# Optimization experiments

Measured on AMD Instinct MI355X. Metric: run time of the kernel, lower is better.

## Reference

```python
import jax, jax.numpy as jnp
import numpy as np

B, C, E, H = 4, 2048, 1024, 16
D = E // H
EPS = 1e-5

def _layernorm(x, g, b):
    mu = jnp.mean(x, axis=-1, keepdims=True)
    var = jnp.mean(jnp.square(x - mu), axis=-1, keepdims=True)
    return (x - mu) * jax.lax.rsqrt(var + EPS) * g + b

def setup_inputs() -> dict:
    key = jax.random.key(0)
    ks = jax.random.split(key, 12)
    s = 1.0 / np.sqrt(E)
    return {
        "inputs": jax.random.normal(ks[0], (B, C, E), dtype=jnp.float32),
        "Wq": jax.random.normal(ks[1], (E, E), dtype=jnp.float32) * s,
        "bq": jnp.zeros((E,), dtype=jnp.float32),
        "Wk": jax.random.normal(ks[2], (E, E), dtype=jnp.float32) * s,
        "bk": jnp.zeros((E,), dtype=jnp.float32),
        "Wv": jax.random.normal(ks[3], (E, E), dtype=jnp.float32) * s,
        "bv": jnp.zeros((E,), dtype=jnp.float32),
        "g1": jnp.ones((E,), dtype=jnp.float32),
        "beta1": jnp.zeros((E,), dtype=jnp.float32),
        "g2": jnp.ones((E,), dtype=jnp.float32),
        "beta2": jnp.zeros((E,), dtype=jnp.float32),
        "W1": jax.random.normal(ks[4], (E, 4 * E), dtype=jnp.float32) * s,
        "bm1": jnp.zeros((4 * E,), dtype=jnp.float32),
        "W2": jax.random.normal(ks[5], (4 * E, E), dtype=jnp.float32) * (1.0 / np.sqrt(4 * E)),
        "bm2": jnp.zeros((E,), dtype=jnp.float32),
    }

def reference(inputs, Wq, bq, Wk, bk, Wv, bv, g1, beta1, g2, beta2, W1, bm1, W2, bm2):
    b, c, e = inputs.shape
    normed = _layernorm(inputs, g1, beta1)
    q = (normed @ Wq + bq).reshape(b, c, H, D).transpose(0, 2, 1, 3)  # [B,H,C,D]
    k = (normed @ Wk + bk).reshape(b, c, H, D).transpose(0, 2, 1, 3)
    v = (normed @ Wv + bv).reshape(b, c, H, D).transpose(0, 2, 1, 3)
    scores = jnp.einsum('bhqd,bhkd->bhqk', q, k) / np.sqrt(D).astype(np.float32)
    causal = jnp.triu(jnp.ones((c, c), dtype=bool), k=1)  # True above diagonal
    scores = jnp.where(causal, -jnp.inf, scores)
    probs = jax.nn.softmax(scores, axis=-1)
    attn = jnp.einsum('bhqk,bhkd->bhqd', probs, v)
    attn = attn.transpose(0, 2, 1, 3).reshape(b, c, e)
    out = inputs + attn
    h = _layernorm(out, g2, beta2)
    mlp = jax.nn.relu(h @ W1 + bm1) @ W2 + bm2
    return out + mlp
```

## Files before the change

kernel.cpp:

```cpp
#include <hip/hip_runtime.h>
#include <math.h>

#define B_ 4
#define C_ 2048
#define E_ 1024
#define H_ 16
#define D_ 64
#define ROWS_ (B_*C_)

typedef __bf16 bf16x8 __attribute__((ext_vector_type(8)));
typedef float f32x4 __attribute__((ext_vector_type(4)));

__device__ __forceinline__ float b2f(unsigned short u) {
  unsigned int x = ((unsigned int)u) << 16;
  return __builtin_bit_cast(float, x);
}
__device__ __forceinline__ unsigned short f2b(float f) {
  unsigned int x = __builtin_bit_cast(unsigned int, f);
  unsigned int r = (x + 0x7FFFu + ((x >> 16) & 1u)) >> 16;
  return (unsigned short)r;
}
__device__ __forceinline__ unsigned short tob(float f) { return f2b(f); }
__device__ __forceinline__ unsigned short tob(unsigned short u) { return u; }
__device__ __forceinline__ void store_out(float* p, float v) { *p = v; }
__device__ __forceinline__ void store_out(unsigned short* p, float v) { *p = f2b(v); }

__device__ __forceinline__ void async16(const void* g, void* l) {
  __builtin_amdgcn_global_load_lds(
      (__attribute__((address_space(1))) unsigned int*)g,
      (__attribute__((address_space(3))) unsigned int*)l, 16, 0, 0);
}

template <typename InT>
__global__ __launch_bounds__(256) void transpose64(
    const InT* __restrict__ in, unsigned short* __restrict__ out,
    int s_in, int s_out, int Hz, long zs_b, long zs_h, long zs_out)
{
  __shared__ unsigned short t[64][65];
  int z = blockIdx.z;
  long ib = (long)(z / Hz) * zs_b + (long)(z % Hz) * zs_h;
  long ob = (long)z * zs_out;
  int r0 = blockIdx.y * 64, c0 = blockIdx.x * 64;
  int lane = threadIdx.x & 63, grp = threadIdx.x >> 6;
  for (int i = grp; i < 64; i += 4)
    t[i][lane] = tob(in[ib + (long)(r0 + i) * s_in + c0 + lane]);
  __syncthreads();
  for (int i = grp; i < 64; i += 4)
    out[ob + (long)(c0 + i) * s_out + r0 + lane] = t[lane][i];
}

__global__ void concat_bias(const float* __restrict__ q,
                            const float* __restrict__ k,
                            const float* __restrict__ v,
                            float* __restrict__ o)
{
  int i = blockIdx.x * 256 + threadIdx.x;
  o[i] = (i < 1024) ? q[i] : (i < 2048) ? k[i - 1024] : v[i - 2048];
}

__global__ __launch_bounds__(256) void ln_kernel(
    const float* __restrict__ xin, const unsigned short* __restrict__ addend,
    const float* __restrict__ g, const float* __restrict__ beta,
    unsigned short* __restrict__ yout, float* __restrict__ out1)
{
  int row = blockIdx.x, tid = threadIdx.x;
  size_t base = (size_t)row * E_ + tid * 4;
  float4 xa = *(const float4*)(xin + base);
  float v0 = xa.x, v1 = xa.y, v2 = xa.z, v3 = xa.w;
  if (addend) {
    ushort4 aa = *(const ushort4*)(addend + base);
    v0 += b2f(aa.x); v1 += b2f(aa.y); v2 += b2f(aa.z); v3 += b2f(aa.w);
  }
  if (out1) {
    *(float4*)(out1 + base) = make_float4(v0, v1, v2, v3);
  }
  float s = v0 + v1 + v2 + v3;
  float sq = v0*v0 + v1*v1 + v2*v2 + v3*v3;
  #pragma unroll
  for (int off = 32; off >= 1; off >>= 1) {
    s  += __shfl_xor(s, off);
    sq += __shfl_xor(sq, off);
  }
  __shared__ float red[8];
  int wid = tid >> 6;
  if ((tid & 63) == 0) { red[wid] = s; red[4 + wid] = sq; }
  __syncthreads();
  s  = red[0] + red[1] + red[2] + red[3];
  sq = red[4] + red[5] + red[6] + red[7];
  float mu = s * (1.0f / E_);
  float var = sq * (1.0f / E_) - mu * mu;
  float rs = rsqrtf(var + 1e-5f);
  float4 ga = *(const float4*)(g + tid * 4);
  float4 ba = *(const float4*)(beta + tid * 4);
  ushort4 o;
  o.x = f2b((v0 - mu) * rs * ga.x + ba.x);
  o.y = f2b((v1 - mu) * rs * ga.y + ba.y);
  o.z = f2b((v2 - mu) * rs * ga.z + ba.z);
  o.w = f2b((v3 - mu) * rs * ga.w + ba.w);
  *(ushort4*)(yout + base) = o;
}

template <typename OutT>
__global__ __launch_bounds__(256) void gemm_bt(
    const unsigned short* __restrict__ A, const unsigned short* __restrict__ Bt,
    const float* __restrict__ bias, const float* __restrict__ resid,
    OutT* __restrict__ Co, int M, int N, int K, int lda, int ldb,
    int relu, size_t zs)
{
  __shared__ __align__(16) unsigned short As[128 * 64];
  __shared__ __align__(16) unsigned short Bs[128 * 64];
  int tid = threadIdx.x, lane = tid & 63, wid = tid >> 6;
  int lane15 = lane & 15, quad = lane >> 4;

  int i = blockIdx.x;
  int xcd = i & 7, s = i >> 3;
  int bn = s >> 3;
  int bm = xcd * 8 + (s & 7);
  size_t koff = (size_t)blockIdx.z * K;
  int z0 = (blockIdx.z == 0);
  Co += (size_t)blockIdx.z * zs;

  int m_lo = (wid & 1) * 64, n_lo = (wid >> 1) * 64;

  f32x4 acc[4][4];
  #pragma unroll
  for (int a = 0; a < 4; ++a)
    #pragma unroll
    for (int bb = 0; bb < 4; ++bb) acc[a][bb] = 0.0f;

  int sr = tid >> 3, sc = tid & 7;
  int scs = (sc ^ (sr & 7)) * 8;
  const unsigned short* Ag = A + koff + (size_t)(bm * 128 + sr) * lda + scs;
  const unsigned short* Bg = Bt + koff + (size_t)(bn * 128 + sr) * ldb + scs;
  unsigned short* Al = &As[wid * 512];
  unsigned short* Bl = &Bs[wid * 512];
  int sw15 = lane15 & 7;

  for (int k0 = 0; k0 < K; k0 += 64) {
    async16(Ag,                     Al);
    async16(Ag + (size_t)32 * lda,  Al + 32 * 64);
    async16(Ag + (size_t)64 * lda,  Al + 64 * 64);
    async16(Ag + (size_t)96 * lda,  Al + 96 * 64);
    async16(Bg,                     Bl);
    async16(Bg + (size_t)32 * ldb,  Bl + 32 * 64);
    async16(Bg + (size_t)64 * ldb,  Bl + 64 * 64);
    async16(Bg + (size_t)96 * ldb,  Bl + 96 * 64);
    Ag += 64; Bg += 64;
    __syncthreads();

    #pragma unroll
    for (int kk = 0; kk < 2; ++kk) {
      bf16x8 af[4], bfr[4];
      int qs = kk * 4 + quad;
      #pragma unroll
      for (int t = 0; t < 4; ++t)
        af[t] = *(const bf16x8*)&As[(m_lo + t * 16 + lane15) * 64 + ((qs ^ sw15) * 8)];
      #pragma unroll
      for (int t = 0; t < 4; ++t)
        bfr[t] = *(const bf16x8*)&Bs[(n_lo + t * 16 + lane15) * 64 + ((qs ^ sw15) * 8)];
      #pragma unroll
      for (int mt = 0; mt < 4; ++mt)
        #pragma unroll
        for (int nt = 0; nt < 4; ++nt)
          acc[mt][nt] = __builtin_amdgcn_mfma_f32_16x16x32_bf16(af[mt], bfr[nt], acc[mt][nt], 0, 0, 0);
    }
    __syncthreads();
  }

  #pragma unroll
  for (int nt = 0; nt < 4; ++nt) {
    int col = bn * 128 + n_lo + nt * 16 + lane15;
    float bv = (bias && z0) ? bias[col] : 0.0f;
    #pragma unroll
    for (int mt = 0; mt < 4; ++mt) {
      int row0 = bm * 128 + m_lo + mt * 16 + quad * 4;
      #pragma unroll
      for (int r = 0; r < 4; ++r) {
        float val = acc[mt][nt][r] + bv;
        if (relu) val = fmaxf(val, 0.0f);
        if (resid && z0) val += resid[(size_t)(row0 + r) * N + col];
        store_out(&Co[(size_t)(row0 + r) * N + col], val);
      }
    }
  }
}

__global__ __launch_bounds__(256) void add2(
    const float* __restrict__ p0, const float* __restrict__ p1,
    float* __restrict__ out)
{
  size_t i = ((size_t)blockIdx.x * 256 + threadIdx.x) * 4;
  float4 a = *(const float4*)(p0 + i);
  float4 b = *(const float4*)(p1 + i);
  *(float4*)(out + i) = make_float4(a.x + b.x, a.y + b.y, a.z + b.z, a.w + b.w);
}

__global__ __launch_bounds__(512) void attn_kernel(
    const unsigned short* __restrict__ qkv, const unsigned short* __restrict__ vt,
    unsigned short* __restrict__ attnb,
    float* __restrict__ opart0, float* __restrict__ opart1,
    float* __restrict__ lpart)
{
  __shared__ __align__(16) unsigned short Klds[64 * 64];
  __shared__ __align__(16) unsigned short Vlds[64 * 64];
  __shared__ __align__(16) unsigned short Plds[8][16 * 72];
  int tid = threadIdx.x, lane = tid & 63, widx = tid >> 6;
  int lane15 = lane & 15, quad = lane >> 4;

  int bx = blockIdx.x;
  int qblk, p, split;
  if (bx < 16) { qblk = 15 - (bx >> 1); p = bx & 1; split = 1; }
  else         { qblk = 23 - bx;        p = 0;      split = 0; }
  int ntiles = 2 * qblk + 2;
  int kt0 = (split && p) ? (qblk + 1) : 0;
  int kt1 = (split && !p) ? (qblk + 1) : ntiles;

  int bh = blockIdx.y;
  int b = bh >> 4, h = bh & 15;
  int q0w = qblk * 128 + widx * 16;

  const float QSCALE = 0.18033688011112042f;
  const unsigned short* qb = qkv + (size_t)(b * C_ + q0w + lane15) * 3072 + h * 64;
  bf16x8 qa0 = *(const bf16x8*)(qb + quad * 8);
  bf16x8 qa1 = *(const bf16x8*)(qb + 32 + quad * 8);
  #pragma unroll
  for (int j = 0; j < 8; ++j) {
    qa0[j] = (__bf16)((float)qa0[j] * QSCALE);
    qa1[j] = (__bf16)((float)qa1[j] * QSCALE);
  }

  float lsum[4];
  f32x4 o[4];
  #pragma unroll
  for (int r = 0; r < 4; ++r) lsum[r] = 0.0f;
  #pragma unroll
  for (int nt = 0; nt < 4; ++nt) o[nt] = 0.0f;

  int sr = tid >> 3, sc = tid & 7, sw = sr & 7;
  const unsigned short* kg = qkv + (size_t)(b * C_ + kt0 * 64 + sr) * 3072 + 1024 + h * 64 + (sc ^ sw) * 8;
  const unsigned short* vg = vt + (size_t)bh * 64 * 2048 + (size_t)sr * 2048 + (sc ^ sw) * 8 + kt0 * 64;
  unsigned short* kl = &Klds[sr * 64 + sc * 8];
  unsigned short* vl = &Vlds[sr * 64 + sc * 8];
  int swr = lane15 & 7;

  for (int kt = kt0; kt < kt1; ++kt) {
    int k0 = kt * 64;
    async16(kg, kl);
    async16(vg, vl);
    kg += (size_t)64 * 3072;
    vg += 64;
    __syncthreads();

    if (k0 <= q0w + 15) {
      f32x4 s[4];
      #pragma unroll
      for (int g = 0; g < 4; ++g) s[g] = 0.0f;
      #pragma unroll
      for (int g = 0; g < 4; ++g) {
        int row = g * 16 + lane15;
        bf16x8 kf0 = *(const bf16x8*)&Klds[row * 64 + ((quad ^ swr) * 8)];
        bf16x8 kf1 = *(const bf16x8*)&Klds[row * 64 + (((4 + quad) ^ swr) * 8)];
        s[g] = __builtin_amdgcn_mfma_f32_16x16x32_bf16(qa0, kf0, s[g], 0, 0, 0);
        s[g] = __builtin_amdgcn_mfma_f32_16x16x32_bf16(qa1, kf1, s[g], 0, 0, 0);
      }

      if (k0 + 63 > q0w) {
        #pragma unroll
        for (int g = 0; g < 4; ++g)
          #pragma unroll
          for (int r = 0; r < 4; ++r)
            if (k0 + g * 16 + lane15 > q0w + quad * 4 + r) s[g][r] = -3.0e38f;
      }

      float pv[4][4];
      #pragma unroll
      for (int g = 0; g < 4; ++g)
        #pragma unroll
        for (int r = 0; r < 4; ++r) pv[g][r] = exp2f(s[g][r]);
      #pragma unroll
      for (int r = 0; r < 4; ++r)
        lsum[r] += (pv[0][r] + pv[1][r]) + (pv[2][r] + pv[3][r]);

      __bf16* prow = (__bf16*)&Plds[widx][0];
      #pragma unroll
      for (int g = 0; g < 4; ++g)
        #pragma unroll
        for (int r = 0; r < 4; ++r)
          prow[(quad * 4 + r) * 72 + g * 16 + lane15] = (__bf16)pv[g][r];
      asm volatile("s_waitcnt lgkmcnt(0)" ::: "memory");
      bf16x8 pa0 = *(const bf16x8*)&Plds[widx][lane15 * 72 + quad * 8];
      bf16x8 pa1 = *(const bf16x8*)&Plds[widx][lane15 * 72 + 32 + quad * 8];

      #pragma unroll
      for (int nt = 0; nt < 4; ++nt) {
        int d = nt * 16 + lane15;
        bf16x8 vf0 = *(const bf16x8*)&Vlds[d * 64 + ((quad ^ swr) * 8)];
        bf16x8 vf1 = *(const bf16x8*)&Vlds[d * 64 + (((4 + quad) ^ swr) * 8)];
        o[nt] = __builtin_amdgcn_mfma_f32_16x16x32_bf16(pa0, vf0, o[nt], 0, 0, 0);
        o[nt] = __builtin_amdgcn_mfma_f32_16x16x32_bf16(pa1, vf1, o[nt], 0, 0, 0);
      }
    }
    __syncthreads();
  }

  #pragma unroll
  for (int off = 1; off <= 8; off <<= 1)
    #pragma unroll
    for (int r = 0; r < 4; ++r)
      lsum[r] += __shfl_xor(lsum[r], off);

  if (!split) {
    float rl[4];
    #pragma unroll
    for (int r = 0; r < 4; ++r) rl[r] = 1.0f / lsum[r];
    #pragma unroll
    for (int nt = 0; nt < 4; ++nt)
      #pragma unroll
      for (int r = 0; r < 4; ++r) {
        float val = o[nt][r] * rl[r];
        attnb[(size_t)(b * C_ + q0w + quad * 4 + r) * E_ + h * 64 + nt * 16 + lane15] = f2b(val);
      }
  } else {
    float* op = p ? opart1 : opart0;
    size_t rbase = (size_t)bh * 1024 + (q0w - 1024) + quad * 4;
    #pragma unroll
    for (int nt = 0; nt < 4; ++nt)
      #pragma unroll
      for (int r = 0; r < 4; ++r)
        op[(rbase + r) * 64 + nt * 16 + lane15] = o[nt][r];
    if (lane15 == 0) {
      float* lp = lpart + (size_t)p * 65536;
      #pragma unroll
      for (int r = 0; r < 4; ++r) lp[rbase + r] = lsum[r];
    }
  }
}

__global__ __launch_bounds__(256) void attn_combine(
    const float* __restrict__ opart0, const float* __restrict__ opart1,
    const float* __restrict__ lpart, unsigned short* __restrict__ attnb)
{
  size_t i = (size_t)blockIdx.x * 256 + threadIdx.x;
  int d = (int)(i & 63);
  size_t rowi = i >> 6;
  int bh = (int)(rowi >> 10), row = (int)(rowi & 1023);
  float ov = opart0[rowi * 64 + d] + opart1[rowi * 64 + d];
  float lv = lpart[rowi] + lpart[65536 + rowi];
  int b = bh >> 4, h = bh & 15;
  attnb[(size_t)(b * C_ + 1024 + row) * E_ + h * 64 + d] = f2b(ov / lv);
}

extern "C" void kernel_launch(void* const* d_in, const int* in_sizes, int n_in,
                              void* d_out, int out_size, void* d_ws, size_t ws_size,
                              hipStream_t stream)
{
  const float* x   = (const float*)d_in[0];
  const float* Wq  = (const float*)d_in[1];
  const float* bq  = (const float*)d_in[2];
  const float* Wk  = (const float*)d_in[3];
  const float* bk  = (const float*)d_in[4];
  const float* Wv  = (const float*)d_in[5];
  const float* bv  = (const float*)d_in[6];
  const float* g1  = (const float*)d_in[7];
  const float* be1 = (const float*)d_in[8];
  const float* g2  = (const float*)d_in[9];
  const float* be2 = (const float*)d_in[10];
  const float* W1  = (const float*)d_in[11];
  const float* bm1 = (const float*)d_in[12];
  const float* W2  = (const float*)d_in[13];
  const float* bm2 = (const float*)d_in[14];

  char* ws = (char*)d_ws;
  float*          part0 = (float*)(ws + 0);
  unsigned short* norm1 = (unsigned short*)(ws + 0);
  unsigned short* wT    = (unsigned short*)(ws + 16777216);
  unsigned short* w1T   = (unsigned short*)(ws + 23068672);
  float*          biasq = (float*)(ws + 39845888);
  unsigned short* qkv   = (unsigned short*)(ws + 39858176);
  unsigned short* vtb   = (unsigned short*)(ws + 90189824);
  unsigned short* mid   = (unsigned short*)(ws + 39858176);
  unsigned short* attnb = (unsigned short*)(ws + 106967040);
  float*          out1  = (float*)(ws + 123744256);
  unsigned short* w2T   = (unsigned short*)(ws + 157298688);
  float*          part1 = (float*)(ws + 165687296);
  float*          opart0 = (float*)(ws + 165687296);
  float*          opart1 = (float*)(ws + 123744256);
  float*          lpartb = (float*)(ws + 0);
  size_t part_zs = ((size_t)165687296) / 4;

  transpose64<float><<<dim3(16, 16, 1), 256, 0, stream>>>(Wq, wT,               1024, 1024, 1, 0, 0, 0);
  transpose64<float><<<dim3(16, 16, 1), 256, 0, stream>>>(Wk, wT + 1024 * 1024, 1024, 1024, 1, 0, 0, 0);
  transpose64<float><<<dim3(16, 16, 1), 256, 0, stream>>>(Wv, wT + 2048 * 1024, 1024, 1024, 1, 0, 0, 0);
  transpose64<float><<<dim3(64, 16, 1), 256, 0, stream>>>(W1, w1T, 4096, 1024, 1, 0, 0, 0);
  transpose64<float><<<dim3(16, 64, 1), 256, 0, stream>>>(W2, w2T, 1024, 4096, 1, 0, 0, 0);
  concat_bias<<<12, 256, 0, stream>>>(bq, bk, bv, biasq);

  ln_kernel<<<ROWS_, 256, 0, stream>>>(x, nullptr, g1, be1, norm1, nullptr);

  gemm_bt<unsigned short><<<dim3(24 * 64, 1, 1), 256, 0, stream>>>(
      norm1, wT, biasq, nullptr, qkv, 8192, 3072, 1024, 1024, 1024, 0, 0);

  transpose64<unsigned short><<<dim3(1, 32, 64), 256, 0, stream>>>(
      qkv + 2048, vtb, 3072, 2048, 16, (long)C_ * 3072, 64, (long)64 * 2048);

  attn_kernel<<<dim3(24, 64), 512, 0, stream>>>(qkv, vtb, attnb, opart0, opart1, lpartb);
  attn_combine<<<16384, 256, 0, stream>>>(opart0, opart1, lpartb, attnb);

  ln_kernel<<<ROWS_, 256, 0, stream>>>(x, attnb, g2, be2, norm1, out1);

  gemm_bt<unsigned short><<<dim3(32 * 64, 1, 1), 256, 0, stream>>>(
      norm1, w1T, bm1, nullptr, mid, 8192, 4096, 1024, 1024, 1024, 1, 0);

  gemm_bt<float><<<dim3(8 * 64, 1, 2), 256, 0, stream>>>(
      mid, w2T, bm2, out1, part0, 8192, 1024, 2048, 4096, 4096, 0, part_zs);
  add2<<<8192, 256, 0, stream>>>(part0, part1, (float*)d_out);
}
```

Before: 552.8 us.

## Replace 128x128 GEMM with double-buffered 256x256 ping-pong pipelined kernel

Replaces the single-buffered 128x128-tile GEMM with a 512-thread 256x256-tile kernel. It double-buffers LDS and interleaves async global-to-LDS loads with MFMA quarters, using explicit waitcnt, barriers and setprio. The goal is to hide load latency behind compute and raise arithmetic intensity per tile. In exchange it needs 128KB of LDS and more registers per block, gives smaller grids (128 blocks x2 for W2), and depends on fragile hand-placed barrier and waitcnt ordering.

```diff
diff --git a/kernel.cpp b/kernel.cpp
--- a/kernel.cpp
+++ b/kernel.cpp
@@ -100,80 +100,150 @@
   *(ushort4*)(yout + base) = o;
 }
 
+#define BARC() { asm volatile("" ::: "memory"); __builtin_amdgcn_s_barrier(); asm volatile("" ::: "memory"); }
+
+#define MFMA_Q(mh, Af, Bf) do {                                             \
+  __builtin_amdgcn_s_setprio(1);                                            \
+  _Pragma("unroll")                                                         \
+  for (int mt_ = 0; mt_ < 4; ++mt_)                                         \
+    _Pragma("unroll")                                                       \
+    for (int nt_ = 0; nt_ < 4; ++nt_)                                       \
+      acc[(mh)*4+mt_][nt_] = __builtin_amdgcn_mfma_f32_16x16x32_bf16(       \
+          Af[(mh)*4+mt_], Bf[nt_], acc[(mh)*4+mt_][nt_], 0, 0, 0);          \
+  __builtin_amdgcn_s_setprio(0);                                            \
+} while (0)
+
 template <typename OutT>
-__global__ __launch_bounds__(256) void gemm_bt(
+__global__ __launch_bounds__(512, 2) void gemm256(
     const unsigned short* __restrict__ A, const unsigned short* __restrict__ Bt,
     const float* __restrict__ bias, const float* __restrict__ resid,
     OutT* __restrict__ Co, int M, int N, int K, int lda, int ldb,
     int relu, size_t zs)
 {
-  __shared__ __align__(16) unsigned short As[128 * 64];
-  __shared__ __align__(16) unsigned short Bs[128 * 64];
+  __shared__ __align__(16) unsigned short As[2][256 * 64];
+  __shared__ __align__(16) unsigned short Bs[2][256 * 64];
   int tid = threadIdx.x, lane = tid & 63, wid = tid >> 6;
   int lane15 = lane & 15, quad = lane >> 4;
+  int wm = wid >> 2, wn = wid & 3;
 
   int i = blockIdx.x;
-  int xcd = i & 7, s = i >> 3;
-  int bn = s >> 3;
-  int bm = xcd * 8 + (s & 7);
+  int xcd = i & 7, c = i >> 3;
+  int bm = xcd * 4 + (c & 3);
+  int bn = c >> 2;
   size_t koff = (size_t)blockIdx.z * K;
   int z0 = (blockIdx.z == 0);
   Co += (size_t)blockIdx.z * zs;
 
-  int m_lo = (wid & 1) * 64, n_lo = (wid >> 1) * 64;
-
-  f32x4 acc[4][4];
-  #pragma unroll
-  for (int a = 0; a < 4; ++a)
-    #pragma unroll
-    for (int bb = 0; bb < 4; ++bb) acc[a][bb] = 0.0f;
-
   int sr = tid >> 3, sc = tid & 7;
   int scs = (sc ^ (sr & 7)) * 8;
-  const unsigned short* Ag = A + koff + (size_t)(bm * 128 + sr) * lda + scs;
-  const unsigned short* Bg = Bt + koff + (size_t)(bn * 128 + sr) * ldb + scs;
-  unsigned short* Al = &As[wid * 512];
-  unsigned short* Bl = &Bs[wid * 512];
-  int sw15 = lane15 & 7;
-
-  for (int k0 = 0; k0 < K; k0 += 64) {
-    async16(Ag,                     Al);
-    async16(Ag + (size_t)32 * lda,  Al + 32 * 64);
-    async16(Ag + (size_t)64 * lda,  Al + 64 * 64);
-    async16(Ag + (size_t)96 * lda,  Al + 96 * 64);
-    async16(Bg,                     Bl);
-    async16(Bg + (size_t)32 * ldb,  Bl + 32 * 64);
-    async16(Bg + (size_t)64 * ldb,  Bl + 64 * 64);
-    async16(Bg + (size_t)96 * ldb,  Bl + 96 * 64);
-    Ag += 64; Bg += 64;
-    __syncthreads();
-
-    #pragma unroll
-    for (int kk = 0; kk < 2; ++kk) {
-      bf16x8 af[4], bfr[4];
-      int qs = kk * 4 + quad;
-      #pragma unroll
-      for (int t = 0; t < 4; ++t)
-        af[t] = *(const bf16x8*)&As[(m_lo + t * 16 + lane15) * 64 + ((qs ^ sw15) * 8)];
-      #pragma unroll
-      for (int t = 0; t < 4; ++t)
-        bfr[t] = *(const bf16x8*)&Bs[(n_lo + t * 16 + lane15) * 64 + ((qs ^ sw15) * 8)];
-      #pragma unroll
-      for (int mt = 0; mt < 4; ++mt)
-        #pragma unroll
-        for (int nt = 0; nt < 4; ++nt)
-          acc[mt][nt] = __builtin_amdgcn_mfma_f32_16x16x32_bf16(af[mt], bfr[nt], acc[mt][nt], 0, 0, 0);
-    }
-    __syncthreads();
+  const unsigned short* Ag = A + koff + (size_t)(bm * 256 + sr) * lda + scs;
+  const unsigned short* Bg = Bt + koff + (size_t)(bn * 256 + sr) * ldb + scs;
+  int dstb = wid * 512;
+
+  int NT = K >> 6;
+
+  f32x4 acc[8][4];
+  #pragma unroll
+  for (int m = 0; m < 8; ++m)
+    #pragma unroll
+    for (int n = 0; n < 4; ++n) acc[m][n] = 0.0f;
+
+  auto stA = [&](int kt, int h) {
+    const unsigned short* s = Ag + (size_t)(h * 128) * lda + kt * 64;
+    unsigned short* d = &As[kt & 1][h * 8192 + dstb];
+    async16(s, d);
+    async16(s + (size_t)64 * lda, d + 4096);
+  };
+  auto stB = [&](int kt, int h) {
+    const unsigned short* s = Bg + (size_t)(h * 128) * ldb + kt * 64;
+    unsigned short* d = &Bs[kt & 1][h * 8192 + dstb];
+    async16(s, d);
+    async16(s + (size_t)64 * ldb, d + 4096);
+  };
+  int rsw = lane15 & 7;
+  auto ldA = [&](int buf, int m, int kk) {
+    int row = wm * 128 + m * 16 + lane15;
+    return *(const bf16x8*)&As[buf][row * 64 + (((kk * 4 + quad) ^ rsw) * 8)];
+  };
+  auto ldB = [&](int buf, int n, int kk) {
+    int row = wn * 64 + n * 16 + lane15;
+    return *(const bf16x8*)&Bs[buf][row * 64 + (((kk * 4 + quad) ^ rsw) * 8)];
+  };
+
+  stA(0, 0); stA(0, 1); stB(0, 0); stB(0, 1);
+  stA(1, 0); stA(1, 1);
+  asm volatile("s_waitcnt vmcnt(4)" ::: "memory");
+  __builtin_amdgcn_s_barrier();
+
+  for (int it = 0; it < (NT >> 1); ++it) {
+    int u = 2 * it;
+    bool more = (u + 2 < NT);
+    bf16x8 a0[8], b0[4], a1[8], b1[4];
+
+    #pragma unroll
+    for (int m = 0; m < 8; ++m) a0[m] = ldA(0, m, 0);
+    #pragma unroll
+    for (int n = 0; n < 4; ++n) b0[n] = ldB(0, n, 0);
+    stB(u + 1, 0);
+    BARC();
+    asm volatile("s_waitcnt lgkmcnt(0)" ::: "memory");
+    MFMA_Q(0, a0, b0);
+    BARC();
+    #pragma unroll
+    for (int m = 0; m < 8; ++m) a1[m] = ldA(0, m, 1);
+    #pragma unroll
+    for (int n = 0; n < 4; ++n) b1[n] = ldB(0, n, 1);
+    stB(u + 1, 1);
+    BARC();
+    asm volatile("s_waitcnt lgkmcnt(0)" ::: "memory");
+    MFMA_Q(1, a0, b0);
+    BARC();
+    if (more) stA(u + 2, 0);
+    BARC();
+    MFMA_Q(0, a1, b1);
+    BARC();
+    if (more) stA(u + 2, 1);
+    BARC();
+    MFMA_Q(1, a1, b1);
+    if (more) { asm volatile("s_waitcnt vmcnt(4)" ::: "memory"); }
+    else      { asm volatile("s_waitcnt vmcnt(0)" ::: "memory"); }
+    BARC();
+    #pragma unroll
+    for (int m = 0; m < 8; ++m) a0[m] = ldA(1, m, 0);
+    #pragma unroll
+    for (int n = 0; n < 4; ++n) b0[n] = ldB(1, n, 0);
+    if (more) stB(u + 2, 0);
+    BARC();
+    asm volatile("s_waitcnt lgkmcnt(0)" ::: "memory");
+    MFMA_Q(0, a0, b0);
+    BARC();
+    #pragma unroll
+    for (int m = 0; m < 8; ++m) a1[m] = ldA(1, m, 1);
+    #pragma unroll
+    for (int n = 0; n < 4; ++n) b1[n] = ldB(1, n, 1);
+    if (more) stB(u + 2, 1);
+    BARC();
+    asm volatile("s_waitcnt lgkmcnt(0)" ::: "memory");
+    MFMA_Q(1, a0, b0);
+    BARC();
+    if (more) stA(u + 3, 0);
+    BARC();
+    MFMA_Q(0, a1, b1);
+    BARC();
+    if (more) stA(u + 3, 1);
+    BARC();
+    MFMA_Q(1, a1, b1);
+    if (more) { asm volatile("s_waitcnt vmcnt(4)" ::: "memory"); }
+    BARC();
   }
 
   #pragma unroll
   for (int nt = 0; nt < 4; ++nt) {
-    int col = bn * 128 + n_lo + nt * 16 + lane15;
+    int col = bn * 256 + wn * 64 + nt * 16 + lane15;
     float bv = (bias && z0) ? bias[col] : 0.0f;
     #pragma unroll
-    for (int mt = 0; mt < 4; ++mt) {
-      int row0 = bm * 128 + m_lo + mt * 16 + quad * 4;
+    for (int mt = 0; mt < 8; ++mt) {
+      int row0 = bm * 256 + wm * 128 + mt * 16 + quad * 4;
       #pragma unroll
       for (int r = 0; r < 4; ++r) {
         float val = acc[mt][nt][r] + bv;
@@ -397,7 +467,7 @@
 
   ln_kernel<<<ROWS_, 256, 0, stream>>>(x, nullptr, g1, be1, norm1, nullptr);
 
-  gemm_bt<unsigned short><<<dim3(24 * 64, 1, 1), 256, 0, stream>>>(
+  gemm256<unsigned short><<<dim3(384, 1, 1), 512, 0, stream>>>(
       norm1, wT, biasq, nullptr, qkv, 8192, 3072, 1024, 1024, 1024, 0, 0);
 
   transpose64<unsigned short><<<dim3(1, 32, 64), 256, 0, stream>>>(
@@ -408,10 +478,10 @@
 
   ln_kernel<<<ROWS_, 256, 0, stream>>>(x, attnb, g2, be2, norm1, out1);
 
-  gemm_bt<unsigned short><<<dim3(32 * 64, 1, 1), 256, 0, stream>>>(
+  gemm256<unsigned short><<<dim3(512, 1, 1), 512, 0, stream>>>(
       norm1, w1T, bm1, nullptr, mid, 8192, 4096, 1024, 1024, 1024, 1, 0);
 
-  gemm_bt<float><<<dim3(8 * 64, 1, 2), 256, 0, stream>>>(
+  gemm256<float><<<dim3(128, 1, 2), 512, 0, stream>>>(
       mid, w2T, bm2, out1, part0, 8192, 1024, 2048, 4096, 4096, 0, part_zs);
   add2<<<8192, 256, 0, stream>>>(part0, part1, (float*)d_out);
 }
```

Result: slower. 763.5 us (+38.1%).
